# Kernel optimization log

Hardware: AMD Instinct MI355X
Metric: run time of the kernel (lower is better)

## Reference

```python
import jax, jax.numpy as jnp
import numpy as np

EPS = 0.01
MAX_ITER = 10
H = W = 48
N = H * W
B = 16


def radial_cost_matrix():
    # pairwise Euclidean distance between pixel coordinates of an HxW grid,
    # normalized to [0, 1]; shape (1, N, N)
    ys, xs = np.meshgrid(np.arange(H), np.arange(W), indexing='ij')
    coords = np.stack([ys.ravel(), xs.ravel()], axis=1).astype(np.float32)  # (N, 2)
    d = np.sqrt(((coords[:, None, :] - coords[None, :, :]) ** 2).sum(-1))
    d = d / d.max()
    return d[None].astype(np.float32)


def setup_inputs() -> dict:
    key = jax.random.key(0)
    k1, k2 = jax.random.split(key)
    pred_logits = jax.random.normal(k1, (B, H, W), dtype=jnp.float32)
    t = jax.random.uniform(k2, (B, H, W), dtype=jnp.float32)
    target_probs = t / t.sum(axis=(1, 2), keepdims=True)  # valid probability maps
    C = jnp.asarray(radial_cost_matrix())  # (1, N, N) buffer, not trainable
    return {"pred_logits": pred_logits, "target_probs": target_probs, "C": C}


def _M(C, u, v):
    # M_ij = (-c_ij + u_i + v_j) / eps ; shapes: C (1,N,N), u,v (B,N) -> (B,N,N)
    return (-C + u[..., None] + v[..., None, :]) / EPS


def reference(pred_logits, target_probs, C):
    b = pred_logits.shape[0]
    pred_logp = jax.nn.log_softmax(pred_logits.reshape(b, -1), axis=1)  # (B, N)
    target_logp = jnp.log(target_probs.reshape(b, -1) + 1e-8)           # (B, N)

    u = jnp.zeros_like(pred_logp)
    v = jnp.zeros_like(target_logp)
    for _ in range(MAX_ITER):  # fixed small iteration count (no early exit)
        u = EPS * (pred_logp - jax.nn.logsumexp(_M(C, u, v), axis=-1)) + u
        v = EPS * (target_logp - jax.nn.logsumexp(_M(C, u, v), axis=-2)) + v

    pi = jnp.exp(_M(C, u, v))                      # (B, N, N) transport plan
    cost = jnp.sum(pi * C, axis=(-2, -1))           # (B,)
    return cost.mean()                              # reduction='mean'
```

## Files before the change

kernel.cpp:

```cpp
#include <hip/hip_runtime.h>


namespace {

constexpr int N    = 2304;
constexpr int B    = 16;
constexpr int NB   = N * B;
constexpr int R    = 10;
constexpr int WIN  = 21;
constexpr int WPAD = 24;
constexpr int APX  = 12;
constexpr int AST  = 76;
constexpr int NOUT = 144;
constexpr int NTH  = WIN * 12;
constexpr int AVR1 = 23;
constexpr int AVR2 = 43;
constexpr int BVR  = 23;
constexpr int PST  = 25;
constexpr int P1L  = 46 * PST;
constexpr int P2L  = 6 * PST;

__device__ __forceinline__ float wave_sum(float v) {
#pragma unroll
    for (int off = 32; off >= 1; off >>= 1) v += __shfl_xor(v, off);
    return v;
}

template <bool WC, int NT>
__device__ __forceinline__ void stage_wt(float* wtl, float* wcl,
                                         const float* __restrict__ C) {
    for (int i = threadIdx.x; i < WIN * WPAD; i += NT) {
        const int dy = i / WPAD, dx = i - dy * WPAD;
        float wv = 0.f, wc = 0.f;
        if (dx < WIN) {
            const float c = C[1176 * N + (14 + dy) * 48 + (14 + dx)];
            wv = __expf(c * -100.f);
            wc = wv * c;
        }
        wtl[i] = wv;
        if (WC) wcl[i] = wc;
    }
}

template <bool ONES, int NT>
__device__ __forceinline__ void stage_ap(float* vl, const float* img,
                                         int b, int ytop, int nrows) {
    for (int i = threadIdx.x; i < nrows * 18; i += NT) {
        const int rr = i / 18, c4 = i - rr * 18;
        const int y = ytop + rr, x0 = c4 * 4 - APX;
        float4 v = make_float4(0.f, 0.f, 0.f, 0.f);
        if ((unsigned)y < 48u && (unsigned)x0 < 48u)
            v = ONES ? make_float4(1.f, 1.f, 1.f, 1.f)
                     : *(const float4*)(img + b * N + y * 48 + x0);
        *(float4*)&vl[rr * AST + c4 * 4] = v;
    }
}

__device__ __forceinline__ void conv_row(const float* vp, const float* wp,
                                         float* acc) {
    float vr[36], wr[24];
#pragma unroll
    for (int c = 0; c < 9; ++c) *(float4*)&vr[4 * c] = *(const float4*)&vp[4 * c];
#pragma unroll
    for (int c = 0; c < 6; ++c) *(float4*)&wr[4 * c] = *(const float4*)&wp[4 * c];
#pragma unroll
    for (int dx = 0; dx < WIN; ++dx)
#pragma unroll
        for (int k = 0; k < 12; ++k)
            acc[k] = fmaf(wr[dx], vr[k + 2 + dx], acc[k]);
}

__device__ __forceinline__ void conv_row24(const float* vp, const float* wp,
                                           float* acc) {
    float vr[48], wr[24];
#pragma unroll
    for (int c = 0; c < 12; ++c) *(float4*)&vr[4 * c] = *(const float4*)&vp[4 * c];
#pragma unroll
    for (int c = 0; c < 6; ++c) *(float4*)&wr[4 * c] = *(const float4*)&wp[4 * c];
#pragma unroll
    for (int dx = 0; dx < WIN; ++dx)
#pragma unroll
        for (int k = 0; k < 24; ++k)
            acc[k] = fmaf(wr[dx], vr[k + 2 + dx], acc[k]);
}

__global__ __launch_bounds__(256) void sk_a1(const float* __restrict__ logits,
                                             const float* __restrict__ C,
                                             float* __restrict__ smstat,
                                             float* __restrict__ A0,
                                             float* __restrict__ out) {
    __shared__ float vl[AVR1 * AST];
    __shared__ float wtl[WIN * WPAD];
    __shared__ float part[NTH * 12];
    __shared__ float sred[8];

    const int bid = blockIdx.x;
    const int b   = bid & 15;
    const int y0  = (bid >> 4) * 3;
    const int tid = threadIdx.x, w = tid >> 6, lane = tid & 63;

    stage_wt<false, 256>(wtl, nullptr, C);
    stage_ap<true, 256>(vl, nullptr, b, y0 - R, AVR1);

    float xs[9];
    float m = -3.0e38f;
#pragma unroll
    for (int s9 = 0; s9 < 9; ++s9) {
        xs[s9] = logits[b * N + s9 * 256 + tid];
        m = fmaxf(m, xs[s9]);
    }
#pragma unroll
    for (int off = 32; off >= 1; off >>= 1) m = fmaxf(m, __shfl_xor(m, off));
    if (lane == 0) sred[w] = m;
    __syncthreads();
    m = fmaxf(fmaxf(sred[0], sred[1]), fmaxf(sred[2], sred[3]));
    float sum = 0.f;
#pragma unroll
    for (int s9 = 0; s9 < 9; ++s9) sum += __expf(xs[s9] - m);
#pragma unroll
    for (int off = 32; off >= 1; off >>= 1) sum += __shfl_xor(sum, off);
    __syncthreads();
    if (lane == 0) sred[4 + w] = sum;
    __syncthreads();
    sum = sred[4] + sred[5] + sred[6] + sred[7];
    const float sm_m = m, sm_inv = 1.f / sum;
    if (tid == 0 && (bid >> 4) == 0) {
        smstat[2 * b]     = sm_m;
        smstat[2 * b + 1] = sm_inv;
        if (b == 0) out[0] = 0.f;
    }
    __syncthreads();

    if (tid < NTH) {
        const int dy = tid / 12, strip = tid - dy * 12;
        const int r = strip >> 2, xw = (strip & 3) * 12;
        float acc[12];
#pragma unroll
        for (int k = 0; k < 12; ++k) acc[k] = 0.f;
        conv_row(&vl[(r + dy) * AST + xw], &wtl[dy * WPAD], acc);
#pragma unroll
        for (int c = 0; c < 3; ++c)
            *(float4*)&part[tid * 12 + 4 * c] = *(float4*)&acc[4 * c];
    }
    __syncthreads();

    if (tid < NOUT) {
        float ssum = 0.f;
#pragma unroll
        for (int d = 0; d < WIN; ++d) ssum += part[d * 144 + tid];
        const int o = b * N + (y0 + tid / 48) * 48 + (tid % 48);
        A0[o] = __expf(logits[o] - sm_m) * sm_inv / ssum;
    }
}

__global__ __launch_bounds__(512) void sk_fused(const float* __restrict__ logits,
                                                const float* __restrict__ target,
                                                const float* __restrict__ C,
                                                const float* __restrict__ smstat,
                                                const float* __restrict__ Ain,
                                                float* __restrict__ Aout) {
    __shared__ float vl[AVR2 * AST];
    __shared__ float bt[BVR * AST];
    __shared__ float part[11 * P1L];
    __shared__ float wtl[WIN * WPAD];

    const int bid = blockIdx.x;
    const int b   = bid & 15;
    const int y0  = (bid >> 4) * 3;
    const int tid = threadIdx.x;

    stage_ap<false, 512>(vl, Ain, b, y0 - 2 * R, AVR2);
    stage_wt<false, 512>(wtl, nullptr, C);
    for (int i = tid; i < (BVR * AST) / 4; i += 512)
        *(float4*)&bt[4 * i] = make_float4(0.f, 0.f, 0.f, 0.f);
    const float sm_m = smstat[2 * b], sm_inv = smstat[2 * b + 1];
    __syncthreads();

    if (tid < 506) {
        const int dy2 = tid / 46, rem = tid - dy2 * 46;
        const int rb = rem >> 1, xg = rem & 1;
        float acc[24];
#pragma unroll
        for (int k = 0; k < 24; ++k) acc[k] = 0.f;
        conv_row24(&vl[(rb + 2 * dy2) * AST + xg * 24],
                   &wtl[(2 * dy2) * WPAD], acc);
        if (dy2 < 10)
            conv_row24(&vl[(rb + 2 * dy2 + 1) * AST + xg * 24],
                       &wtl[(2 * dy2 + 1) * WPAD], acc);
        float* pp = &part[dy2 * P1L + (rb * 2 + xg) * PST];
#pragma unroll
        for (int k = 0; k < 24; ++k) pp[k] = acc[k];
    }
    __syncthreads();

    for (int o = tid; o < BVR * 48; o += 512) {
        const int rb = o / 48, x = o - rb * 48;
        const int slot = rb * 2 + (x >= 24 ? 1 : 0);
        const int k = x >= 24 ? x - 24 : x;
        float s = 0.f;
#pragma unroll
        for (int d = 0; d < 11; ++d) s += part[d * P1L + slot * PST + k];
        const int ybg = y0 - R + rb;
        if ((unsigned)ybg < 48u)
            bt[rb * AST + APX + x] = (target[b * N + ybg * 48 + x] + 1e-8f) / s;
    }
    __syncthreads();

    if (tid < 66) {
        const int dy2 = tid / 6, rem = tid - dy2 * 6;
        const int ra = rem >> 1, xg = rem & 1;
        float acc[24];
#pragma unroll
        for (int k = 0; k < 24; ++k) acc[k] = 0.f;
        conv_row24(&bt[(ra + 2 * dy2) * AST + xg * 24],
                   &wtl[(2 * dy2) * WPAD], acc);
        if (dy2 < 10)
            conv_row24(&bt[(ra + 2 * dy2 + 1) * AST + xg * 24],
                       &wtl[(2 * dy2 + 1) * WPAD], acc);
        float* pp = &part[dy2 * P2L + (ra * 2 + xg) * PST];
#pragma unroll
        for (int k = 0; k < 24; ++k) pp[k] = acc[k];
    }
    __syncthreads();

    if (tid < NOUT) {
        const int ra = tid / 48, x = tid - ra * 48;
        const int slot = ra * 2 + (x >= 24 ? 1 : 0);
        const int k = x >= 24 ? x - 24 : x;
        float ssum = 0.f;
#pragma unroll
        for (int d = 0; d < 11; ++d) ssum += part[d * P2L + slot * PST + k];
        const int o = b * N + (y0 + ra) * 48 + x;
        Aout[o] = __expf(logits[o] - sm_m) * sm_inv / ssum;
    }
}

__global__ __launch_bounds__(256) void sk_cost(const float* __restrict__ target,
                                               const float* __restrict__ C,
                                               const float* __restrict__ Ain,
                                               float* __restrict__ out) {
    __shared__ float vl[AVR1 * AST];
    __shared__ float wtl[WIN * WPAD], wcl[WIN * WPAD];
    __shared__ float p1[NTH * 12], p2[NTH * 12];
    __shared__ float sred[4];

    const int bid = blockIdx.x;
    const int b   = bid & 15;
    const int y0  = (bid >> 4) * 3;
    const int tid = threadIdx.x, w = tid >> 6, lane = tid & 63;

    stage_wt<true, 256>(wtl, wcl, C);
    stage_ap<false, 256>(vl, Ain, b, y0 - R, AVR1);
    __syncthreads();

    if (tid < NTH) {
        const int dy = tid / 12, strip = tid - dy * 12;
        const int r = strip >> 2, xw = (strip & 3) * 12;
        float a1[12], a2[12];
#pragma unroll
        for (int k = 0; k < 12; ++k) { a1[k] = 0.f; a2[k] = 0.f; }
        float vr[36], wr[24], cr[24];
        const float* vp = &vl[(r + dy) * AST + xw];
#pragma unroll
        for (int c = 0; c < 9; ++c)
            *(float4*)&vr[4 * c] = *(const float4*)&vp[4 * c];
#pragma unroll
        for (int c = 0; c < 6; ++c) {
            *(float4*)&wr[4 * c] = *(const float4*)&wtl[dy * WPAD + 4 * c];
            *(float4*)&cr[4 * c] = *(const float4*)&wcl[dy * WPAD + 4 * c];
        }
#pragma unroll
        for (int dx = 0; dx < WIN; ++dx)
#pragma unroll
            for (int k = 0; k < 12; ++k) {
                a1[k] = fmaf(wr[dx], vr[k + 2 + dx], a1[k]);
                a2[k] = fmaf(cr[dx], vr[k + 2 + dx], a2[k]);
            }
#pragma unroll
        for (int c = 0; c < 3; ++c) {
            *(float4*)&p1[tid * 12 + 4 * c] = *(float4*)&a1[4 * c];
            *(float4*)&p2[tid * 12 + 4 * c] = *(float4*)&a2[4 * c];
        }
    }
    __syncthreads();

    float val = 0.f;
    if (tid < NOUT) {
        float s1 = 0.f, s2 = 0.f;
#pragma unroll
        for (int d = 0; d < WIN; ++d) {
            s1 += p1[d * 144 + tid];
            s2 += p2[d * 144 + tid];
        }
        const int o = b * N + (y0 + tid / 48) * 48 + (tid % 48);
        val = (target[o] + 1e-8f) / s1 * s2;
    }
    val = wave_sum(val);
    if (lane == 0) sred[w] = val;
    __syncthreads();
    if (tid == 0)
        atomicAdd(out, (sred[0] + sred[1] + sred[2] + sred[3]) * (1.f / 16.f));
}

}

extern "C" void kernel_launch(void* const* d_in, const int* in_sizes, int n_in,
                              void* d_out, int out_size, void* d_ws, size_t ws_size,
                              hipStream_t stream) {
    const float* logits = (const float*)d_in[0];
    const float* target = (const float*)d_in[1];
    const float* C      = (const float*)d_in[2];
    float* out = (float*)d_out;
    float* ws  = (float*)d_ws;

    float* smstat = ws;
    float* A0     = ws + 32;
    float* A1     = A0 + NB;

    sk_a1<<<256, 256, 0, stream>>>(logits, C, smstat, A0, out);

    float* bufs[2] = {A0, A1};
    for (int t = 0; t < 9; ++t) {
        sk_fused<<<256, 512, 0, stream>>>(logits, target, C, smstat,
                                          bufs[t & 1], bufs[(t & 1) ^ 1]);
    }

    sk_cost<<<256, 256, 0, stream>>>(target, C, A1, out);
}
```

Measured before the change: 83.79 us.

## Fuse three half-iteration convolutions per launch with symmetric-weight row pairing

Each kernel launch now performs three chained separable-window convolution passes (a row scaling, then a column scaling, then another) instead of two, using wider halos of 63, 43 and 23 rows. The eighteen half-steps therefore take six launches instead of nine, and a template parameter alternates which marginal feeds each stage. The kernel also exploits the vertical symmetry of the window weights by summing mirrored rows before the FMA loop, which roughly halves the multiply work per pass. The cost is extra redundant halo computation per block, larger shared memory per block that may lower occupancy, and a final buffer change to A0.

```diff
diff --git a/kernel.cpp b/kernel.cpp
--- a/kernel.cpp
+++ b/kernel.cpp
@@ -14,11 +14,12 @@
 constexpr int NOUT = 144;
 constexpr int NTH  = WIN * 12;
 constexpr int AVR1 = 23;
-constexpr int AVR2 = 43;
-constexpr int BVR  = 23;
-constexpr int PST  = 25;
-constexpr int P1L  = 46 * PST;
-constexpr int P2L  = 6 * PST;
+constexpr int V0R  = 63;
+constexpr int T1R  = 43;
+constexpr int T2R  = 23;
+constexpr int P1S  = 2408;
+constexpr int P2S  = 1288;
+constexpr int P3S  = 240;
 
 __device__ __forceinline__ float wave_sum(float v) {
 #pragma unroll
@@ -56,7 +57,7 @@
     }
 }
 
-__device__ __forceinline__ void conv_row(const float* vp, const float* wp,
+__device__ __forceinline__ void conv_c12(const float* vp, const float* wp,
                                          float* acc) {
     float vr[36], wr[24];
 #pragma unroll
@@ -69,12 +70,51 @@
         for (int k = 0; k < 12; ++k)
             acc[k] = fmaf(wr[dx], vr[k + 2 + dx], acc[k]);
 }
-
-__device__ __forceinline__ void conv_row24(const float* vp, const float* wp,
-                                           float* acc) {
+__device__ __forceinline__ void conv_p12(const float* lo, const float* hi,
+                                         const float* wp, float* acc) {
+    float vr[36], wr[24];
+#pragma unroll
+    for (int c = 0; c < 9; ++c) {
+        const float4 a = *(const float4*)&lo[4 * c];
+        const float4 b = *(const float4*)&hi[4 * c];
+        vr[4 * c]     = a.x + b.x;
+        vr[4 * c + 1] = a.y + b.y;
+        vr[4 * c + 2] = a.z + b.z;
+        vr[4 * c + 3] = a.w + b.w;
+    }
+#pragma unroll
+    for (int c = 0; c < 6; ++c) *(float4*)&wr[4 * c] = *(const float4*)&wp[4 * c];
+#pragma unroll
+    for (int dx = 0; dx < WIN; ++dx)
+#pragma unroll
+        for (int k = 0; k < 12; ++k)
+            acc[k] = fmaf(wr[dx], vr[k + 2 + dx], acc[k]);
+}
+__device__ __forceinline__ void conv_c24(const float* vp, const float* wp,
+                                         float* acc) {
     float vr[48], wr[24];
 #pragma unroll
     for (int c = 0; c < 12; ++c) *(float4*)&vr[4 * c] = *(const float4*)&vp[4 * c];
+#pragma unroll
+    for (int c = 0; c < 6; ++c) *(float4*)&wr[4 * c] = *(const float4*)&wp[4 * c];
+#pragma unroll
+    for (int dx = 0; dx < WIN; ++dx)
+#pragma unroll
+        for (int k = 0; k < 24; ++k)
+            acc[k] = fmaf(wr[dx], vr[k + 2 + dx], acc[k]);
+}
+__device__ __forceinline__ void conv_p24(const float* lo, const float* hi,
+                                         const float* wp, float* acc) {
+    float vr[48], wr[24];
+#pragma unroll
+    for (int c = 0; c < 12; ++c) {
+        const float4 a = *(const float4*)&lo[4 * c];
+        const float4 b = *(const float4*)&hi[4 * c];
+        vr[4 * c]     = a.x + b.x;
+        vr[4 * c + 1] = a.y + b.y;
+        vr[4 * c + 2] = a.z + b.z;
+        vr[4 * c + 3] = a.w + b.w;
+    }
 #pragma unroll
     for (int c = 0; c < 6; ++c) *(float4*)&wr[4 * c] = *(const float4*)&wp[4 * c];
 #pragma unroll
@@ -137,7 +177,7 @@
         float acc[12];
 #pragma unroll
         for (int k = 0; k < 12; ++k) acc[k] = 0.f;
-        conv_row(&vl[(r + dy) * AST + xw], &wtl[dy * WPAD], acc);
+        conv_c12(&vl[(r + dy) * AST + xw], &wtl[dy * WPAD], acc);
 #pragma unroll
         for (int c = 0; c < 3; ++c)
             *(float4*)&part[tid * 12 + 4 * c] = *(float4*)&acc[4 * c];
@@ -153,85 +193,133 @@
     }
 }
 
-__global__ __launch_bounds__(512) void sk_fused(const float* __restrict__ logits,
-                                                const float* __restrict__ target,
-                                                const float* __restrict__ C,
-                                                const float* __restrict__ smstat,
-                                                const float* __restrict__ Ain,
-                                                float* __restrict__ Aout) {
-    __shared__ float vl[AVR2 * AST];
-    __shared__ float bt[BVR * AST];
-    __shared__ float part[11 * P1L];
+template <int PAR>
+__global__ __launch_bounds__(512) void sk_triple(const float* __restrict__ logits,
+                                                 const float* __restrict__ target,
+                                                 const float* __restrict__ C,
+                                                 const float* __restrict__ smstat,
+                                                 const float* __restrict__ Ain,
+                                                 float* __restrict__ Aout) {
+    __shared__ float vl0[V0R * AST];
+    __shared__ float t1[T1R * AST];
+    __shared__ float t2[T2R * AST];
     __shared__ float wtl[WIN * WPAD];
+    __shared__ float part[6 * P1S];
 
     const int bid = blockIdx.x;
     const int b   = bid & 15;
     const int y0  = (bid >> 4) * 3;
     const int tid = threadIdx.x;
 
-    stage_ap<false, 512>(vl, Ain, b, y0 - 2 * R, AVR2);
+    stage_ap<false, 512>(vl0, Ain, b, y0 - 30, V0R);
     stage_wt<false, 512>(wtl, nullptr, C);
-    for (int i = tid; i < (BVR * AST) / 4; i += 512)
-        *(float4*)&bt[4 * i] = make_float4(0.f, 0.f, 0.f, 0.f);
+    for (int i = tid; i < T1R * AST; i += 512) t1[i] = 0.f;
+    for (int i = tid; i < T2R * AST; i += 512) t2[i] = 0.f;
     const float sm_m = smstat[2 * b], sm_inv = smstat[2 * b + 1];
     __syncthreads();
 
-    if (tid < 506) {
-        const int dy2 = tid / 46, rem = tid - dy2 * 46;
-        const int rb = rem >> 1, xg = rem & 1;
+    for (int tau = tid; tau < 516; tau += 512) {
+        const int uc = tau / 86, slot = tau - uc * 86;
+        const int rb = slot >> 1, xw = (slot & 1) * 24;
         float acc[24];
 #pragma unroll
         for (int k = 0; k < 24; ++k) acc[k] = 0.f;
-        conv_row24(&vl[(rb + 2 * dy2) * AST + xg * 24],
-                   &wtl[(2 * dy2) * WPAD], acc);
-        if (dy2 < 10)
-            conv_row24(&vl[(rb + 2 * dy2 + 1) * AST + xg * 24],
-                       &wtl[(2 * dy2 + 1) * WPAD], acc);
-        float* pp = &part[dy2 * P1L + (rb * 2 + xg) * PST];
-#pragma unroll
-        for (int k = 0; k < 24; ++k) pp[k] = acc[k];
-    }
-    __syncthreads();
-
-    for (int o = tid; o < BVR * 48; o += 512) {
-        const int rb = o / 48, x = o - rb * 48;
-        const int slot = rb * 2 + (x >= 24 ? 1 : 0);
+        if (uc == 0) {
+            conv_c24(&vl0[(rb + 10) * AST + xw], &wtl[10 * WPAD], acc);
+            conv_p24(&vl0[(rb + 9) * AST + xw], &vl0[(rb + 11) * AST + xw],
+                     &wtl[11 * WPAD], acc);
+        } else if (uc < 5) {
+            const int d = 2 * uc;
+            conv_p24(&vl0[(rb + 10 - d) * AST + xw],
+                     &vl0[(rb + 10 + d) * AST + xw], &wtl[(10 + d) * WPAD], acc);
+            conv_p24(&vl0[(rb + 9 - d) * AST + xw],
+                     &vl0[(rb + 11 + d) * AST + xw], &wtl[(11 + d) * WPAD], acc);
+        } else {
+            conv_p24(&vl0[rb * AST + xw], &vl0[(rb + 20) * AST + xw],
+                     &wtl[20 * WPAD], acc);
+        }
+        float* pp = &part[uc * P1S + slot * 28];
+#pragma unroll
+        for (int c = 0; c < 6; ++c) *(float4*)&pp[4 * c] = *(float4*)&acc[4 * c];
+    }
+    __syncthreads();
+
+    for (int o = tid; o < T1R * 48; o += 512) {
+        const int rt = o / 48, x = o - rt * 48;
+        const int slot = rt * 2 + (x >= 24 ? 1 : 0);
         const int k = x >= 24 ? x - 24 : x;
         float s = 0.f;
 #pragma unroll
-        for (int d = 0; d < 11; ++d) s += part[d * P1L + slot * PST + k];
-        const int ybg = y0 - R + rb;
-        if ((unsigned)ybg < 48u)
-            bt[rb * AST + APX + x] = (target[b * N + ybg * 48 + x] + 1e-8f) / s;
-    }
-    __syncthreads();
-
-    if (tid < 66) {
-        const int dy2 = tid / 6, rem = tid - dy2 * 6;
-        const int ra = rem >> 1, xg = rem & 1;
+        for (int l = 0; l < 6; ++l) s += part[l * P1S + slot * 28 + k];
+        const int y = y0 - 20 + rt;
+        if ((unsigned)y < 48u) {
+            const int g = b * N + y * 48 + x;
+            const float sv = (PAR == 0) ? (target[g] + 1e-8f)
+                                        : __expf(logits[g] - sm_m) * sm_inv;
+            t1[rt * AST + APX + x] = sv / s;
+        }
+    }
+    __syncthreads();
+
+    if (tid < 506) {
+        const int u = tid / 46, slot = tid - u * 46;
+        const int rt2 = slot >> 1, xw = (slot & 1) * 24;
         float acc[24];
 #pragma unroll
         for (int k = 0; k < 24; ++k) acc[k] = 0.f;
-        conv_row24(&bt[(ra + 2 * dy2) * AST + xg * 24],
-                   &wtl[(2 * dy2) * WPAD], acc);
-        if (dy2 < 10)
-            conv_row24(&bt[(ra + 2 * dy2 + 1) * AST + xg * 24],
-                       &wtl[(2 * dy2 + 1) * WPAD], acc);
-        float* pp = &part[dy2 * P2L + (ra * 2 + xg) * PST];
-#pragma unroll
-        for (int k = 0; k < 24; ++k) pp[k] = acc[k];
+        if (u == 0) conv_c24(&t1[(rt2 + 10) * AST + xw], &wtl[10 * WPAD], acc);
+        else        conv_p24(&t1[(rt2 + 10 - u) * AST + xw],
+                             &t1[(rt2 + 10 + u) * AST + xw],
+                             &wtl[(10 + u) * WPAD], acc);
+        float* pp = &part[u * P2S + slot * 28];
+#pragma unroll
+        for (int c = 0; c < 6; ++c) *(float4*)&pp[4 * c] = *(float4*)&acc[4 * c];
+    }
+    __syncthreads();
+
+    for (int o = tid; o < T2R * 48; o += 512) {
+        const int rt = o / 48, x = o - rt * 48;
+        const int slot = rt * 2 + (x >= 24 ? 1 : 0);
+        const int k = x >= 24 ? x - 24 : x;
+        float s = 0.f;
+#pragma unroll
+        for (int l = 0; l < 11; ++l) s += part[l * P2S + slot * 28 + k];
+        const int y = y0 - 10 + rt;
+        if ((unsigned)y < 48u) {
+            const int g = b * N + y * 48 + x;
+            const float sv = (PAR == 0) ? __expf(logits[g] - sm_m) * sm_inv
+                                        : (target[g] + 1e-8f);
+            t2[rt * AST + APX + x] = sv / s;
+        }
+    }
+    __syncthreads();
+
+    if (tid < 132) {
+        const int u = tid / 12, slot = tid - u * 12;
+        const int ra = slot >> 2, xw = (slot & 3) * 12;
+        float acc[12];
+#pragma unroll
+        for (int k = 0; k < 12; ++k) acc[k] = 0.f;
+        if (u == 0) conv_c12(&t2[(ra + 10) * AST + xw], &wtl[10 * WPAD], acc);
+        else        conv_p12(&t2[(ra + 10 - u) * AST + xw],
+                             &t2[(ra + 10 + u) * AST + xw],
+                             &wtl[(10 + u) * WPAD], acc);
+        float* pp = &part[u * P3S + slot * 20];
+#pragma unroll
+        for (int c = 0; c < 3; ++c) *(float4*)&pp[4 * c] = *(float4*)&acc[4 * c];
     }
     __syncthreads();
 
     if (tid < NOUT) {
         const int ra = tid / 48, x = tid - ra * 48;
-        const int slot = ra * 2 + (x >= 24 ? 1 : 0);
-        const int k = x >= 24 ? x - 24 : x;
-        float ssum = 0.f;
-#pragma unroll
-        for (int d = 0; d < 11; ++d) ssum += part[d * P2L + slot * PST + k];
-        const int o = b * N + (y0 + ra) * 48 + x;
-        Aout[o] = __expf(logits[o] - sm_m) * sm_inv / ssum;
+        const int slot = ra * 4 + x / 12, k = x % 12;
+        float s = 0.f;
+#pragma unroll
+        for (int l = 0; l < 11; ++l) s += part[l * P3S + slot * 20 + k];
+        const int g = b * N + (y0 + ra) * 48 + x;
+        const float sv = (PAR == 0) ? (target[g] + 1e-8f)
+                                    : __expf(logits[g] - sm_m) * sm_inv;
+        Aout[g] = sv / s;
     }
 }
 
@@ -320,10 +408,14 @@
     sk_a1<<<256, 256, 0, stream>>>(logits, C, smstat, A0, out);
 
     float* bufs[2] = {A0, A1};
-    for (int t = 0; t < 9; ++t) {
-        sk_fused<<<256, 512, 0, stream>>>(logits, target, C, smstat,
-                                          bufs[t & 1], bufs[(t & 1) ^ 1]);
-    }
-
-    sk_cost<<<256, 256, 0, stream>>>(target, C, A1, out);
-}
+    for (int t = 0; t < 6; ++t) {
+        if ((t & 1) == 0)
+            sk_triple<0><<<256, 512, 0, stream>>>(logits, target, C, smstat,
+                                                  bufs[t & 1], bufs[(t + 1) & 1]);
+        else
+            sk_triple<1><<<256, 512, 0, stream>>>(logits, target, C, smstat,
+                                                  bufs[t & 1], bufs[(t + 1) & 1]);
+    }
+
+    sk_cost<<<256, 256, 0, stream>>>(target, C, A0, out);
+}
```

Result: slower. 123.7 us (+47.6%).
